# Optimization experiments

Hardware: AMD Instinct MI355X
Metric: run time of the kernel (lower is better)

## Reference

```python
import jax, jax.numpy as jnp
import numpy as np

B, N, D = 128, 64, 20
H, WM = 256, 4
CAUG = D + 1                      # time-augmented path channels
SIG = CAUG + CAUG * (CAUG - 1) // 2   # depth-2 log-signature channels = 231
C = SIG + 1                       # time-augmented control channels = 232
EPS = 1e-5


def _ln(x, g, b):
    m = jnp.mean(x, -1, keepdims=True)
    v = jnp.var(x, -1, keepdims=True)
    return (x - m) * jax.lax.rsqrt(v + EPS) * g + b


def setup_inputs():
    key = jax.random.key(0)
    ks = jax.random.split(key, 12)
    w = lambda k, s: (jax.random.normal(k, s) * 0.02).astype(jnp.float32)
    z = lambda s: jnp.zeros(s, jnp.float32)
    o = lambda s: jnp.ones(s, jnp.float32)
    return dict(
        x=jax.random.normal(ks[0], (B, N, D), jnp.float32),
        hW1=w(ks[1], (D, H)), hb1=z(H), hW2=w(ks[2], (H, H)), hb2=z(H),
        fW1=w(ks[3], (H, WM * H)), fb1=z(WM * H), g1=o(WM * H), be1=z(WM * H),
        fW2=w(ks[4], (WM * H, H)), fb2=z(H), g2=o(H), be2=z(H),
        fW3=w(ks[5], (H, H)), fb3=z(H),
        fW4=w(ks[6], (H, H * C)), fb4=z(H * C),
        yW1=w(ks[7], (H, H // 2)), yb1=z(H // 2), yW2=w(ks[8], (H // 2, 1)), yb2=z(1),
        zW1=w(ks[9], (H, H)), zb1=z(H), zW2=w(ks[10], (H, D)), zb2=z(D),
        sg=o(SIG), sb=z(SIG),
    )


def _forward(x, hW1, hb1, hW2, hb2, fW1, fb1, g1, be1, fW2, fb2, g2, be2,
             fW3, fb3, fW4, fb4, yW1, yb1, yW2, yb2, zW1, zb1, zW2, zb2, sg, sb):
    t = jnp.linspace(0.0, 1.0, N).astype(x.dtype)
    # --- depth-2 streamed log-signature of time-augmented path, basepoint 0 ---
    p = jnp.concatenate([jnp.broadcast_to(t[None, :, None], (B, N, 1)), x], -1)  # (B,N,CAUG)
    prev = jnp.concatenate([jnp.zeros((B, 1, CAUG), x.dtype), p[:, :-1]], 1)
    d = p - prev                                          # piecewise-linear segment increments
    term = prev[..., :, None] * d[..., None, :] - d[..., :, None] * prev[..., None, :]
    levy = 0.5 * jnp.cumsum(term, axis=1)                 # Levy areas, (B,N,CAUG,CAUG)
    iu, ju = np.triu_indices(CAUG, 1)
    logsig = jnp.concatenate([p, levy[:, :, iu, ju]], -1)  # level-1 + level-2 log-sig, (B,N,SIG)
    logsig = _ln(logsig, sg, sb)                          # sig_norm
    # --- natural cubic spline of time-augmented control ---
    y = jnp.concatenate([jnp.broadcast_to(t[None, :, None], (B, N, 1)), logsig], -1)  # (B,N,C)
    h = 1.0 / (N - 1)
    A = np.zeros((N, N), np.float32)
    A[0, 0] = A[-1, -1] = 1.0
    for i in range(1, N - 1):
        A[i, i - 1] = h / 6.0
        A[i, i] = 2.0 * h / 3.0
        A[i, i + 1] = h / 6.0
    rhs = jnp.concatenate([jnp.zeros((B, 1, C), y.dtype),
                           (y[:, 2:] - 2.0 * y[:, 1:-1] + y[:, :-2]) / h,
                           jnp.zeros((B, 1, C), y.dtype)], 1)
    M = jnp.linalg.solve(jnp.asarray(A), rhs.transpose(1, 0, 2).reshape(N, B * C))
    M = M.reshape(N, B, C).transpose(1, 0, 2)             # natural-spline second derivatives
    dy = (y[:, 1:] - y[:, :-1]) / h
    d_knot = dy - (h / 6.0) * (2.0 * M[:, :-1] + M[:, 1:])   # dX/dt at left knots, (B,N-1,C)
    d_mid = dy + (h / 24.0) * (M[:, :-1] - M[:, 1:])         # dX/dt at segment midpoints
    # --- initial hidden state ---
    h0 = jax.nn.relu(x[:, 0] @ hW1 + hb1) @ hW2 + hb2

    def vf(zz):  # RDEFunc MLP -> (B,H,C)
        a = jax.nn.relu(_ln(zz @ fW1 + fb1, g1, be1))
        a = jax.nn.relu(_ln(a @ fW2 + fb2, g2, be2))
        a = jax.nn.relu(a @ fW3 + fb3)
        return (a @ fW4 + fb4).reshape(B, H, C)

    def g(zz, dX):
        return jnp.einsum('bhc,bc->bh', vf(zz), dX)

    def step(zz, dd):  # explicit midpoint step of dz = F(z) dX/dt dt
        dk, dm = dd
        k1 = g(zz, dk)
        zn = zz + h * g(zz + 0.5 * h * k1, dm)
        return zn, zn

    _, hs = jax.lax.scan(step, h0, (d_knot.transpose(1, 0, 2), d_mid.transpose(1, 0, 2)))
    hT = hs[-1]                                            # terminal hidden (return_path=False)
    Y = jax.nn.relu(hT @ yW1 + yb1) @ yW2 + yb2
    Z = jax.nn.relu(hT @ zW1 + zb1) @ zW2 + zb2
    return Y, Z, hT


def reference(x, hW1, hb1, hW2, hb2, fW1, fb1, g1, be1, fW2, fb2, g2, be2,
              fW3, fb3, fW4, fb4, yW1, yb1, yW2, yb2, zW1, zb1, zW2, zb2, sg, sb):
    return _forward(x, hW1, hb1, hW2, hb2, fW1, fb1, g1, be1, fW2, fb2, g2, be2,
                    fW3, fb3, fW4, fb4, yW1, yb1, yW2, yb2, zW1, zb1, zW2, zb2, sg, sb)
```

## Files before the change

### kernel.cpp

```cpp
#include <hip/hip_runtime.h>

#define B 128
#define N 64
#define D 20
#define H 256
#define WMH 1024
#define CAUG 21
#define SIG 231
#define C 232
#define CP 240
#define KA 288
#define NSEG 63
#define NPH 126
#define HSTEP (1.0f/63.0f)
#define EPS 1e-5f

typedef __attribute__((ext_vector_type(8))) short short8;
typedef __attribute__((ext_vector_type(4))) float f32x4;
typedef __attribute__((ext_vector_type(4))) unsigned int uint4v;
typedef __attribute__((ext_vector_type(2))) int int2v;
typedef __attribute__((ext_vector_type(4))) int int4v;
typedef unsigned int uint;

__device__ inline short f2bf(float f) {
  uint u = __float_as_uint(f);
  uint r = (u + 0x7fffu + ((u >> 16) & 1u)) >> 16;
  return (short)r;
}
__device__ inline float bf2f(short h) {
  return __uint_as_float(((uint)(unsigned short)h) << 16);
}
#define MFMA16(a, b, c) __builtin_amdgcn_mfma_f32_16x16x32_bf16((a), (b), (c), 0, 0, 0)

__device__ inline void cstoreu(uint* p, uint v) {
  __hip_atomic_store(p, v, __ATOMIC_RELAXED, __HIP_MEMORY_SCOPE_AGENT);
}
__device__ inline void cstoref(float* p, float v) {
  __hip_atomic_store(p, v, __ATOMIC_RELAXED, __HIP_MEMORY_SCOPE_AGENT);
}
__device__ inline void cstorei(int* p, int v) {
  __hip_atomic_store(p, v, __ATOMIC_RELAXED, __HIP_MEMORY_SCOPE_AGENT);
}

#define CLOAD8(r0,r1,r2,r3,r4,r5,r6,r7,addr)                                   \
  asm volatile("global_load_dwordx4 %0, %8, off sc0 sc1\n\t"                   \
               "global_load_dwordx4 %1, %8, off offset:16 sc0 sc1\n\t"         \
               "global_load_dwordx4 %2, %8, off offset:128 sc0 sc1\n\t"        \
               "global_load_dwordx4 %3, %8, off offset:144 sc0 sc1\n\t"        \
               "global_load_dwordx4 %4, %8, off offset:256 sc0 sc1\n\t"        \
               "global_load_dwordx4 %5, %8, off offset:272 sc0 sc1\n\t"        \
               "global_load_dwordx4 %6, %8, off offset:384 sc0 sc1\n\t"        \
               "global_load_dwordx4 %7, %8, off offset:400 sc0 sc1\n\t"        \
               "s_waitcnt vmcnt(0)"                                            \
               : "=&v"(r0), "=&v"(r1), "=&v"(r2), "=&v"(r3),                   \
                 "=&v"(r4), "=&v"(r5), "=&v"(r6), "=&v"(r7)                    \
               : "v"(addr)                                                     \
               : "memory")

#define CLOAD2(r0,r1,addr)                                                     \
  asm volatile("global_load_dwordx4 %0, %2, off sc0 sc1\n\t"                   \
               "global_load_dwordx4 %1, %2, off offset:16 sc0 sc1\n\t"         \
               "s_waitcnt vmcnt(0)"                                            \
               : "=&v"(r0), "=&v"(r1) : "v"(addr) : "memory")

#define CLOADB2(r0,r1,a0,a1)                                                   \
  asm volatile("global_load_dwordx4 %0, %2, off sc0 sc1\n\t"                   \
               "global_load_dwordx4 %1, %3, off sc0 sc1\n\t"                   \
               "s_waitcnt vmcnt(0)"                                            \
               : "=&v"(r0), "=&v"(r1) : "v"(a0), "v"(a1) : "memory")

#define CLOAD9(r0,r1,r2,r3,r4,r5,r6,r7,r8,a0,a1,a2,a3,a4,a5,a6,a7,a8)          \
  asm volatile("global_load_dwordx4 %0, %9, off sc0 sc1\n\t"                   \
               "global_load_dwordx4 %1, %10, off sc0 sc1\n\t"                  \
               "global_load_dwordx4 %2, %11, off sc0 sc1\n\t"                  \
               "global_load_dwordx4 %3, %12, off sc0 sc1\n\t"                  \
               "global_load_dwordx4 %4, %13, off sc0 sc1\n\t"                  \
               "global_load_dwordx4 %5, %14, off sc0 sc1\n\t"                  \
               "global_load_dwordx4 %6, %15, off sc0 sc1\n\t"                  \
               "global_load_dwordx4 %7, %16, off sc0 sc1\n\t"                  \
               "global_load_dwordx4 %8, %17, off sc0 sc1\n\t"                  \
               "s_waitcnt vmcnt(0)"                                            \
               : "=&v"(r0), "=&v"(r1), "=&v"(r2), "=&v"(r3), "=&v"(r4),        \
                 "=&v"(r5), "=&v"(r6), "=&v"(r7), "=&v"(r8)                    \
               : "v"(a0), "v"(a1), "v"(a2), "v"(a3), "v"(a4), "v"(a5),         \
                 "v"(a6), "v"(a7), "v"(a8)                                     \
               : "memory")

__device__ inline void post(int* w, int v) {
  __builtin_amdgcn_fence(__ATOMIC_RELEASE, "workgroup");
  __syncthreads();
  if (threadIdx.x == 0) cstorei(w, v);
}
__device__ inline void poll16(const int* f, int tgt) {
  if (threadIdx.x < 64) {
    const int* p = f + (threadIdx.x & 15);
    for (;;) {
      int v;
      asm volatile("global_load_dword %0, %1, off sc0 sc1\n\ts_waitcnt vmcnt(0)"
                   : "=v"(v) : "v"(p) : "memory");
      if (__all(v >= tgt)) break;
      __builtin_amdgcn_s_sleep(1);
    }
  }
  __builtin_amdgcn_fence(__ATOMIC_ACQUIRE, "workgroup");
  __syncthreads();
}
__device__ inline void poll128(const int* f, int tgt) {
  if (threadIdx.x < 64) {
    const int* p = f + threadIdx.x * 2;
    for (;;) {
      int2v v;
      asm volatile("global_load_dwordx2 %0, %1, off sc0 sc1\n\ts_waitcnt vmcnt(0)"
                   : "=v"(v) : "v"(p) : "memory");
      if (__all(v[0] >= tgt && v[1] >= tgt)) break;
      __builtin_amdgcn_s_sleep(1);
    }
  }
  __builtin_amdgcn_fence(__ATOMIC_ACQUIRE, "workgroup");
  __syncthreads();
}
__device__ inline void poll256(const int* f, int tgt) {
  if (threadIdx.x < 64) {
    const int* p = f + threadIdx.x * 4;
    for (;;) {
      int4v v;
      asm volatile("global_load_dwordx4 %0, %1, off sc0 sc1\n\ts_waitcnt vmcnt(0)"
                   : "=v"(v) : "v"(p) : "memory");
      if (__all(v[0] >= tgt && v[1] >= tgt && v[2] >= tgt && v[3] >= tgt)) break;
      __builtin_amdgcn_s_sleep(1);
    }
  }
  __builtin_amdgcn_fence(__ATOMIC_ACQUIRE, "workgroup");
  __syncthreads();
}

__device__ inline void unpk(uint4v a, uint4v b, short8& ah, short8& al) {
#pragma unroll
  for (int e = 0; e < 4; e++) {
    ah[e]     = (short)(a[e] >> 16); al[e]     = (short)(a[e] & 0xffffu);
    ah[4 + e] = (short)(b[e] >> 16); al[4 + e] = (short)(b[e] & 0xffffu);
  }
}

__global__ __launch_bounds__(256) void k_logsig(const float* __restrict__ x,
                                                const float* __restrict__ sg,
                                                const float* __restrict__ sb,
                                                float* __restrict__ y) {
  __shared__ float yb[N][C];
  int b = blockIdx.x, tid = threadIdx.x;
  for (int ii = tid; ii < N * CAUG; ii += 256) {
    int n = ii / CAUG, j = ii % CAUG;
    float v = (j == 0) ? (n * (1.0f / 63.0f)) : x[(b * N + n) * D + (j - 1)];
    yb[n][1 + j] = v;
  }
  __syncthreads();
  if (tid < 210) {
    int i = 0, rem = tid;
    while (rem >= (CAUG - 1) - i) { rem -= (CAUG - 1) - i; i++; }
    int j = i + 1 + rem;
    float acc = 0.f, pi_prev = 0.f, pj_prev = 0.f;
    for (int n = 0; n < N; n++) {
      float pi = yb[n][1 + i], pj = yb[n][1 + j];
      float di = pi - pi_prev, dj = pj - pj_prev;
      acc += 0.5f * (pi_prev * dj - di * pj_prev);
      yb[n][1 + CAUG + tid] = acc;
      pi_prev = pi; pj_prev = pj;
    }
  }
  __syncthreads();
  int w = tid >> 6, l = tid & 63;
  for (int n = w; n < N; n += 4) {
    float s1 = 0.f, s2 = 0.f;
    for (int s = l; s < SIG; s += 64) { float v = yb[n][1 + s]; s1 += v; s2 += v * v; }
    for (int off = 32; off > 0; off >>= 1) { s1 += __shfl_down(s1, off); s2 += __shfl_down(s2, off); }
    s1 = __shfl(s1, 0); s2 = __shfl(s2, 0);
    float mean = s1 * (1.0f / SIG);
    float var  = s2 * (1.0f / SIG) - mean * mean;
    float rs = rsqrtf(var + EPS);
    float* yrow = y + ((size_t)b * N + n) * C;
    if (l == 0) yrow[0] = n * (1.0f / 63.0f);
    for (int s = l; s < SIG; s += 64)
      yrow[1 + s] = (yb[n][1 + s] - mean) * rs * sg[s] + sb[s];
  }
}

__global__ __launch_bounds__(256) void k_spline(const float* __restrict__ y,
                                                float* __restrict__ dknot,
                                                float* __restrict__ dmid) {
  __shared__ float yb[N * C];
  __shared__ float cp_s[62], id_s[62];
  int b = blockIdx.x, tid = threadIdx.x;
  for (int ii = tid; ii < N * C; ii += 256) yb[ii] = y[(size_t)b * N * C + ii];
  if (tid == 0) {
    const float a = HSTEP / 6.f, bb = 2.f * HSTEP / 3.f;
    float id0 = 1.f / bb; id_s[0] = id0; cp_s[0] = a * id0;
    for (int j = 1; j < 62; j++) {
      float den = bb - a * cp_s[j - 1];
      float idj = 1.f / den; id_s[j] = idj; cp_s[j] = a * idj;
    }
  }
  __syncthreads();
  int c = tid;
  if (c >= 232 && c < CP) {
    for (int n = 0; n < NSEG; n++) {
      dknot[((size_t)n * B + b) * CP + c] = 0.f;
      dmid [((size_t)n * B + b) * CP + c] = 0.f;
    }
  } else if (c < 232) {
    const float a = HSTEP / 6.f;
    float dp[62];
    dp[0] = (yb[2 * C + c] - 2.f * yb[1 * C + c] + yb[0 * C + c]) * 63.0f * id_s[0];
#pragma unroll
    for (int j = 1; j < 62; j++) {
      float rj = (yb[(j + 2) * C + c] - 2.f * yb[(j + 1) * C + c] + yb[j * C + c]) * 63.0f;
      dp[j] = (rj - a * dp[j - 1]) * id_s[j];
    }
#pragma unroll
    for (int j = 60; j >= 0; j--) dp[j] -= cp_s[j] * dp[j + 1];
#pragma unroll
    for (int n = 0; n < NSEG; n++) {
      float Mn  = (n == 0)  ? 0.f : dp[n - 1];
      float Mn1 = (n == 62) ? 0.f : dp[n];
      float dy = (yb[(n + 1) * C + c] - yb[n * C + c]) * 63.0f;
      dknot[((size_t)n * B + b) * CP + c] = dy - (HSTEP / 6.f)  * (2.f * Mn + Mn1);
      dmid [((size_t)n * B + b) * CP + c] = dy + (HSTEP / 24.f) * (Mn - Mn1);
    }
  }
}

__global__ __launch_bounds__(256) void k_h0(const float* __restrict__ x,
                                            const float* __restrict__ hW1,
                                            const float* __restrict__ hb1,
                                            const float* __restrict__ hW2,
                                            const float* __restrict__ hb2,
                                            float* __restrict__ z,
                                            uint* __restrict__ Xu) {
  __shared__ float r[H];
  int b = blockIdx.x, tid = threadIdx.x;
  float s = hb1[tid];
#pragma unroll
  for (int d = 0; d < D; d++) s += x[(size_t)(b * N) * D + d] * hW1[d * H + tid];
  r[tid] = fmaxf(s, 0.f);
  __syncthreads();
  float s2 = hb2[tid];
  for (int k = 0; k < H; k++) s2 += r[k] * hW2[k * H + tid];
  z[b * H + tid] = s2;
  short hi = f2bf(s2);
  short lo = f2bf(s2 - bf2f(hi));
  Xu[b * H + tid] = ((uint)(unsigned short)hi << 16) | (unsigned short)lo;
}

__global__ __launch_bounds__(256) void k_prep_t(const float* __restrict__ fW4,
                                                short* __restrict__ W4T) {
  __shared__ float tile[64][65];
  int m0 = blockIdx.x * 64, k0 = blockIdx.y * 64;
  int lane = threadIdx.x & 63, wr = threadIdx.x >> 6;
#pragma unroll
  for (int j = 0; j < 16; j++) {
    int kk = wr * 16 + j;
    tile[kk][lane] = fW4[(size_t)(k0 + kk) * 59392 + m0 + lane];
  }
  __syncthreads();
#pragma unroll
  for (int j = 0; j < 16; j++) {
    int mloc = wr * 16 + j;
    int m = m0 + mloc;
    int hh = m / 232, cc = m - hh * 232;
    W4T[((size_t)hh * CP + cc) * KA + k0 + lane] = f2bf(tile[lane][mloc]);
  }
}

__global__ __launch_bounds__(256) void k_prep_pad(const float* __restrict__ fb4,
                                                  short* __restrict__ W4T) {
  int idx = blockIdx.x * 256 + threadIdx.x;
  const int partA = 61440 * 32;
  if (idx < partA) {
    int row = idx >> 5, j = idx & 31;
    int hh = row / CP, cc = row - hh * CP;
    short v = 0;
    if (j == 0 && cc < 232) v = f2bf(fb4[hh * 232 + cc]);
    W4T[(size_t)row * KA + 256 + j] = v;
  } else {
    int t = idx - partA;
    int k = t & 255; t >>= 8;
    int cc = 232 + (t & 7); int hh = t >> 3;
    W4T[((size_t)hh * CP + cc) * KA + k] = 0;
  }
}

__global__ __launch_bounds__(256) void k_prep_wt(const float* __restrict__ in,
                                                 short* __restrict__ out,
                                                 int K, int Nn) {
  __shared__ float tile[64][65];
  int n0 = blockIdx.x * 64, k0 = blockIdx.y * 64;
  int lane = threadIdx.x & 63, wr = threadIdx.x >> 6;
#pragma unroll
  for (int j = 0; j < 16; j++) {
    int kk = wr * 16 + j;
    tile[kk][lane] = in[(size_t)(k0 + kk) * Nn + n0 + lane];
  }
  __syncthreads();
#pragma unroll
  for (int j = 0; j < 16; j++) {
    int nl = wr * 16 + j;
    out[(size_t)(n0 + nl) * K + k0 + lane] = f2bf(tile[lane][nl]);
  }
}

__global__ __launch_bounds__(128) void k_prep_t3pad(short* __restrict__ t3aug) {
  int r = threadIdx.x;
  if (r < 128) {
    int base = ((r >> 4) * 9 + 8) * 64 + (r & 15);
#pragma unroll
    for (int q = 0; q < 4; q++)
#pragma unroll
      for (int j = 0; j < 8; j++)
        t3aug[(size_t)(base + q * 16) * 8 + j] = (q == 0 && j == 0) ? (short)0x3F80 : (short)0;
  }
}

__global__ __launch_bounds__(256) void k_prep_zero(int* __restrict__ p, int n) {
  int i = blockIdx.x * 256 + threadIdx.x;
  if (i < n) p[i] = 0;
}

__global__ __launch_bounds__(512, 1) void k_scan(
    const short* __restrict__ W1T, const float* __restrict__ fb1,
    const float* __restrict__ g1,  const float* __restrict__ be1,
    const short* __restrict__ W2T, const float* __restrict__ fb2,
    const float* __restrict__ g2,  const float* __restrict__ be2,
    const short* __restrict__ W3T, const float* __restrict__ fb3,
    const short* __restrict__ W4T,
    const float* __restrict__ dknot, const float* __restrict__ dmid,
    float* __restrict__ z, uint* __restrict__ Xu, uint* __restrict__ t3u,
    float* __restrict__ T1, float* __restrict__ T2,
    int* __restrict__ flags) {
  const int blk = blockIdx.x;
  const int tid = threadIdx.x;
  const int wave = tid >> 6, lane = tid & 63;
  const int lm = lane & 15, q = lane >> 4;
  const int m = (blk & 127) >> 4;
  const int n = blk & 15;
  const int ks = wave >> 2, nwt = wave & 3;
  const int wv2 = (wave + n) & 7;
  const int wv3 = (wave + n) & 7;

  __shared__ short t3s[B * KA];
  __shared__ float red2[8][256];
  __shared__ float red4[8][128];
  __shared__ float zcol[128];
  __shared__ float g1s[WMH], be1s[WMH];
  __shared__ float g2s[H], be2s[H];
  __shared__ float fb1s[64];
  __shared__ float fb2s[16], fb3s[16];
  __shared__ uint xs[16 * 260];

  int* eS1 = flags;
  int* eS2 = flags + 128;
  int* eS3 = flags + 256;
  int* eS4 = flags + 384;

  const int nts = (wave < 7) ? 2 : 1;
  const int nt0 = wave * 2;
  short8 bfr[2][9];
  for (int t = 0; t < nts; t++) {
    const short* wp = W4T + ((size_t)blk * CP + (nt0 + t) * 16 + lm) * KA + q * 8;
#pragma unroll
    for (int kc = 0; kc < 9; kc++)
      bfr[t][kc] = *(const short8*)(wp + kc * 32);
  }
  short8 w1f[4], w2f[4], w3f;
  if (blk < 128) {
    const short* p1 = W1T + ((size_t)(n * 64 + nwt * 16 + lm)) * H + ks * 128 + q * 8;
#pragma unroll
    for (int kc = 0; kc < 4; kc++) w1f[kc] = *(const short8*)(p1 + kc * 32);
    const short* p2 = W2T + ((size_t)(n * 16 + lm)) * WMH + wv2 * 128 + q * 8;
#pragma unroll
    for (int kc = 0; kc < 4; kc++) w2f[kc] = *(const short8*)(p2 + kc * 32);
    w3f = *(const short8*)(W3T + ((size_t)(n * 16 + lm)) * H + wv3 * 32 + q * 8);
  }
  for (int i = tid; i < WMH; i += 512) { g1s[i] = g1[i]; be1s[i] = be1[i]; }
  for (int i = tid; i < H; i += 512)   { g2s[i] = g2[i]; be2s[i] = be2[i]; }
  if (tid < 64) fb1s[tid] = fb1[n * 64 + tid];
  if (tid < 16) { fb2s[tid] = fb2[n * 16 + tid]; fb3s[tid] = fb3[n * 16 + tid]; }
  if (tid < 128) zcol[tid] = z[(size_t)tid * H + blk];
  __syncthreads();

#pragma unroll 1
  for (int p = 0; p < NPH; p++) {
    const int seg = p >> 1, pm = p & 1;
    const float* dX = (pm ? dmid : dknot) + (size_t)seg * B * CP;
    const float scale = pm ? HSTEP : 0.5f * HSTEP;

    if (blk < 128) {
      if (p) poll256(eS4, p);
      {
        const uint* xsrc = Xu + (size_t)(m * 16) * H;
        int j0 = tid * 4, j1 = (tid + 512) * 4;
        uint4v v0, v1;
        CLOADB2(v0, v1, xsrc + j0, xsrc + j1);
        *(uint4v*)&xs[(j0 >> 8) * 260 + (j0 & 255)] = v0;
        *(uint4v*)&xs[(j1 >> 8) * 260 + (j1 & 255)] = v1;
      }
      __syncthreads();
      {
        f32x4 acc = {0.f, 0.f, 0.f, 0.f};
        const int xb = lm * 260 + ks * 128 + q * 8;
#pragma unroll
        for (int kc = 0; kc < 4; kc++) {
          uint4v a = *(const uint4v*)&xs[xb + kc * 32];
          uint4v b = *(const uint4v*)&xs[xb + kc * 32 + 4];
          short8 ah, al;
          unpk(a, b, ah, al);
          acc = MFMA16(ah, w1f[kc], acc);
          acc = MFMA16(al, w1f[kc], acc);
        }
#pragma unroll
        for (int r = 0; r < 4; r++) red2[wave][(q * 4 + r) * 16 + lm] = acc[r];
      }
      __syncthreads();
      if (wave < 4) {
        int col = n * 64 + wave * 16 + lm;
        float fb = fb1s[wave * 16 + lm];
#pragma unroll
        for (int r = 0; r < 4; r++) {
          int idx = (q * 4 + r) * 16 + lm;
          float v = red2[wave][idx] + red2[wave + 4][idx] + fb;
          cstoref(T1 + (size_t)(m * 16 + q * 4 + r) * WMH + col, v);
        }
      }
      post(eS1 + m * 16 + n, p + 1);

      poll16(eS1 + m * 16, p + 1);
      const float* tp = T1 + (size_t)(m * 16 + lm) * WMH + wv2 * 128 + q * 8;
      uint4v yv[8];
      CLOAD8(yv[0], yv[1], yv[2], yv[3], yv[4], yv[5], yv[6], yv[7], tp);
      {
        float s = 0.f, ss = 0.f;
#pragma unroll
        for (int i = 0; i < 8; i++)
#pragma unroll
          for (int e = 0; e < 4; e++) {
            float v = __uint_as_float(yv[i][e]);
            s += v; ss += v * v;
          }
        s += __shfl_xor(s, 16); ss += __shfl_xor(ss, 16);
        s += __shfl_xor(s, 32); ss += __shfl_xor(ss, 32);
        if (q == 0) { red2[wave][lm] = s; red2[wave][16 + lm] = ss; }
        __syncthreads();
        float S = 0.f, SS = 0.f;
#pragma unroll
        for (int w = 0; w < 8; w++) { S += red2[w][lm]; SS += red2[w][16 + lm]; }
        float mean = S * (1.f / WMH);
        float var  = SS * (1.f / WMH) - mean * mean;
        float rsv  = rsqrtf(var + EPS);
        __syncthreads();
        f32x4 acc = {0.f, 0.f, 0.f, 0.f};
#pragma unroll
        for (int kc = 0; kc < 4; kc++) {
          int kg = wv2 * 128 + kc * 32 + q * 8;
          short8 ah, al;
#pragma unroll
          for (int jj = 0; jj < 8; jj++) {
            float v = __uint_as_float(yv[kc * 2 + (jj >> 2)][jj & 3]);
            float a = fmaxf((v - mean) * rsv * g1s[kg + jj] + be1s[kg + jj], 0.f);
            short hi = f2bf(a);
            ah[jj] = hi;
            al[jj] = f2bf(a - bf2f(hi));
          }
          acc = MFMA16(ah, w2f[kc], acc);
          acc = MFMA16(al, w2f[kc], acc);
        }
#pragma unroll
        for (int r = 0; r < 4; r++) red2[wave][(q * 4 + r) * 16 + lm] = acc[r];
      }
      __syncthreads();
      if (tid < 256) {
        int ri = tid >> 4, ci = tid & 15;
        float v = fb2s[ci];
#pragma unroll
        for (int w = 0; w < 8; w++) v += red2[w][tid];
        cstoref(T2 + (size_t)(m * 16 + ri) * H + n * 16 + ci, v);
      }
      post(eS2 + m * 16 + n, p + 1);

      poll16(eS2 + m * 16, p + 1);
      const float* t2p = T2 + (size_t)(m * 16 + lm) * H + wv3 * 32 + q * 8;
      uint4v u0, u1;
      CLOAD2(u0, u1, t2p);
      {
        float s = 0.f, ss = 0.f;
#pragma unroll
        for (int e = 0; e < 4; e++) {
          float v0 = __uint_as_float(u0[e]), v1 = __uint_as_float(u1[e]);
          s += v0 + v1; ss += v0 * v0 + v1 * v1;
        }
        s += __shfl_xor(s, 16); ss += __shfl_xor(ss, 16);
        s += __shfl_xor(s, 32); ss += __shfl_xor(ss, 32);
        if (q == 0) { red2[wave][lm] = s; red2[wave][16 + lm] = ss; }
        __syncthreads();
        float S = 0.f, SS = 0.f;
#pragma unroll
        for (int w = 0; w < 8; w++) { S += red2[w][lm]; SS += red2[w][16 + lm]; }
        float mean = S * (1.f / H);
        float var  = SS * (1.f / H) - mean * mean;
        float rsv  = rsqrtf(var + EPS);
        __syncthreads();
        int kg = wv3 * 32 + q * 8;
        short8 ah, al;
#pragma unroll
        for (int jj = 0; jj < 8; jj++) {
          float v = __uint_as_float((jj < 4 ? u0[jj & 3] : u1[jj & 3]));
          float a = fmaxf((v - mean) * rsv * g2s[kg + jj] + be2s[kg + jj], 0.f);
          short hi = f2bf(a);
          ah[jj] = hi;
          al[jj] = f2bf(a - bf2f(hi));
        }
        f32x4 acc = {0.f, 0.f, 0.f, 0.f};
        acc = MFMA16(ah, w3f, acc);
        acc = MFMA16(al, w3f, acc);
#pragma unroll
        for (int r = 0; r < 4; r++) red2[wave][(q * 4 + r) * 16 + lm] = acc[r];
      }
      __syncthreads();
      if (tid < 256) {
        int ri = tid >> 4, ci = tid & 15;
        float v = fb3s[ci];
#pragma unroll
        for (int w = 0; w < 8; w++) v += red2[w][tid];
        v = fmaxf(v, 0.f);
        float vo = __shfl_xor(v, 1);
        if ((ci & 1) == 0) {
          int kglob = n * 16 + ci;
          int d = (m * 9 + (kglob >> 5)) * 64 + ((kglob >> 3) & 3) * 16 + ri;
          uint u = ((uint)(unsigned short)f2bf(vo) << 16)
                 | (unsigned short)f2bf(v);
          cstoreu(t3u + d * 4 + ((kglob & 7) >> 1), u);
        }
      }
      post(eS3 + m * 16 + n, p + 1);
    } else {
      if (p + 1 < NPH) {
        const int seg2 = (p + 1) >> 1, pm2 = (p + 1) & 1;
        const float* dX2 = (pm2 ? dmid : dknot) + (size_t)seg2 * B * CP;
        int i0 = tid * 64;
        if (i0 > B * CP - 64) i0 = B * CP - 64;
        int i1 = i0 + 32;
        float t0, t1;
        asm volatile("global_load_dword %0, %2, off\n\t"
                     "global_load_dword %1, %3, off\n\t"
                     "s_waitcnt vmcnt(0)"
                     : "=&v"(t0), "=&v"(t1)
                     : "v"(dX2 + i0), "v"(dX2 + i1) : "memory");
        asm volatile("" :: "v"(t0), "v"(t1));
      }
    }

    {
      poll128(eS3, p + 1);
      {
        int s0 = blk % 9;
        int s1 = s0 + 1 >= 9 ? s0 + 1 - 9 : s0 + 1;
        int s2 = s1 + 1 >= 9 ? s1 + 1 - 9 : s1 + 1;
        int s3 = s2 + 1 >= 9 ? s2 + 1 - 9 : s2 + 1;
        int s4 = s3 + 1 >= 9 ? s3 + 1 - 9 : s3 + 1;
        int s5 = s4 + 1 >= 9 ? s4 + 1 - 9 : s4 + 1;
        int s6 = s5 + 1 >= 9 ? s5 + 1 - 9 : s5 + 1;
        int s7 = s6 + 1 >= 9 ? s6 + 1 - 9 : s6 + 1;
        int s8 = s7 + 1 >= 9 ? s7 + 1 - 9 : s7 + 1;
        const uint* tb = t3u + tid * 4;
        uint4v r0, r1, r2, r3, r4, r5, r6, r7, r8;
        CLOAD9(r0, r1, r2, r3, r4, r5, r6, r7, r8,
               tb + s0 * 2048, tb + s1 * 2048, tb + s2 * 2048,
               tb + s3 * 2048, tb + s4 * 2048, tb + s5 * 2048,
               tb + s6 * 2048, tb + s7 * 2048, tb + s8 * 2048);
        *(uint4v*)(t3s + (size_t)s0 * 4096 + tid * 8) = r0;
        *(uint4v*)(t3s + (size_t)s1 * 4096 + tid * 8) = r1;
        *(uint4v*)(t3s + (size_t)s2 * 4096 + tid * 8) = r2;
        *(uint4v*)(t3s + (size_t)s3 * 4096 + tid * 8) = r3;
        *(uint4v*)(t3s + (size_t)s4 * 4096 + tid * 8) = r4;
        *(uint4v*)(t3s + (size_t)s5 * 4096 + tid * 8) = r5;
        *(uint4v*)(t3s + (size_t)s6 * 4096 + tid * 8) = r6;
        *(uint4v*)(t3s + (size_t)s7 * 4096 + tid * 8) = r7;
        *(uint4v*)(t3s + (size_t)s8 * 4096 + tid * 8) = r8;
      }
      __syncthreads();
      for (int mm = 0; mm < 8; mm++) {
        short8 afr[9];
#pragma unroll
        for (int kc = 0; kc < 9; kc++)
          afr[kc] = *(const short8*)(t3s + (size_t)((mm * 9 + kc) * 64 + lane) * 8);
        f32x4 acc0 = {0.f, 0.f, 0.f, 0.f}, acc1 = {0.f, 0.f, 0.f, 0.f};
#pragma unroll
        for (int kc = 0; kc < 9; kc++) {
          acc0 = MFMA16(afr[kc], bfr[0][kc], acc0);
          if (nts > 1) acc1 = MFMA16(afr[kc], bfr[1][kc], acc1);
        }
        float part[4];
#pragma unroll
        for (int r = 0; r < 4; r++) {
          int row = mm * 16 + q * 4 + r;
          float pv = acc0[r] * dX[(size_t)row * CP + nt0 * 16 + lm];
          if (nts > 1) pv += acc1[r] * dX[(size_t)row * CP + (nt0 + 1) * 16 + lm];
          part[r] = pv;
        }
#pragma unroll
        for (int r = 0; r < 4; r++) {
          part[r] += __shfl_xor(part[r], 1);
          part[r] += __shfl_xor(part[r], 2);
          part[r] += __shfl_xor(part[r], 4);
          part[r] += __shfl_xor(part[r], 8);
        }
        if (lm == 0) {
#pragma unroll
          for (int r = 0; r < 4; r++) red4[wave][mm * 16 + q * 4 + r] = part[r];
        }
      }
      __syncthreads();
      if (tid < 128) {
        int row = tid;
        float s = 0.f;
#pragma unroll
        for (int w = 0; w < 8; w++) s += red4[w][row];
        float zo = zcol[row] + scale * s;
        if (pm) zcol[row] = zo;
        if (p == NPH - 1) z[(size_t)row * H + blk] = zo;
        short hi = f2bf(zo);
        short lo = f2bf(zo - bf2f(hi));
        cstoreu(Xu + (size_t)row * H + blk,
                ((uint)(unsigned short)hi << 16) | (unsigned short)lo);
      }
      post(eS4 + blk, p + 1);
    }
  }
}

__global__ __launch_bounds__(256) void k_final(const float* __restrict__ z,
    const float* __restrict__ yW1, const float* __restrict__ yb1,
    const float* __restrict__ yW2, const float* __restrict__ yb2,
    const float* __restrict__ zW1, const float* __restrict__ zb1,
    const float* __restrict__ zW2, const float* __restrict__ zb2,
    float* __restrict__ out) {
  __shared__ float ht[H];
  __shared__ float ry[128];
  __shared__ float rz[H];
  int b = blockIdx.x, tid = threadIdx.x;
  ht[tid] = z[(size_t)b * H + tid];
  __syncthreads();
  if (tid < 128) {
    float s = yb1[tid];
    for (int k = 0; k < H; k++) s += ht[k] * yW1[k * 128 + tid];
    ry[tid] = fmaxf(s, 0.f);
  }
  {
    float s = zb1[tid];
    for (int k = 0; k < H; k++) s += ht[k] * zW1[k * H + tid];
    rz[tid] = fmaxf(s, 0.f);
  }
  __syncthreads();
  if (tid < 64) {
    float sv = ry[tid] * yW2[tid] + ry[tid + 64] * yW2[tid + 64];
    for (int off = 32; off > 0; off >>= 1) sv += __shfl_down(sv, off);
    if (tid == 0) out[b] = sv + yb2[0];
  }
  if (tid < D) {
    float s = zb2[tid];
    for (int k = 0; k < H; k++) s += rz[k] * zW2[k * D + tid];
    out[B + b * D + tid] = s;
  }
  out[B + B * D + (size_t)b * H + tid] = ht[tid];
}

extern "C" void kernel_launch(void* const* d_in, const int* in_sizes, int n_in,
                              void* d_out, int out_size, void* d_ws, size_t ws_size,
                              hipStream_t stream) {
  const float* x   = (const float*)d_in[0];
  const float* hW1 = (const float*)d_in[1];
  const float* hb1 = (const float*)d_in[2];
  const float* hW2 = (const float*)d_in[3];
  const float* hb2 = (const float*)d_in[4];
  const float* fW1 = (const float*)d_in[5];
  const float* fb1 = (const float*)d_in[6];
  const float* g1  = (const float*)d_in[7];
  const float* be1 = (const float*)d_in[8];
  const float* fW2 = (const float*)d_in[9];
  const float* fb2 = (const float*)d_in[10];
  const float* g2  = (const float*)d_in[11];
  const float* be2 = (const float*)d_in[12];
  const float* fW3 = (const float*)d_in[13];
  const float* fb3 = (const float*)d_in[14];
  const float* fW4 = (const float*)d_in[15];
  const float* fb4 = (const float*)d_in[16];
  const float* yW1 = (const float*)d_in[17];
  const float* yb1 = (const float*)d_in[18];
  const float* yW2 = (const float*)d_in[19];
  const float* yb2 = (const float*)d_in[20];
  const float* zW1 = (const float*)d_in[21];
  const float* zb1 = (const float*)d_in[22];
  const float* zW2 = (const float*)d_in[23];
  const float* zb2 = (const float*)d_in[24];
  const float* sg  = (const float*)d_in[25];
  const float* sb  = (const float*)d_in[26];

  float* ws     = (float*)d_ws;
  float* dknot  = ws;
  float* dmid   = dknot + (size_t)NSEG * B * CP;
  float* z      = dmid + (size_t)NSEG * B * CP;
  float* T1     = z + B * H;
  float* T2     = T1 + B * WMH;
  uint* Xu      = (uint*)(T2 + B * H);
  uint* t3u     = Xu + B * H;
  int* flags    = (int*)(t3u + B * KA / 2);
  short* w1T    = (short*)(flags + 1024);
  short* w2T    = w1T + H * WMH;
  short* w3T    = w2T + H * WMH;
  short* W4T    = w3T + H * H;
  float* y      = (float*)W4T;

  hipLaunchKernelGGL(k_logsig, dim3(B), dim3(256), 0, stream, x, sg, sb, y);
  hipLaunchKernelGGL(k_spline, dim3(B), dim3(256), 0, stream, y, dknot, dmid);
  hipLaunchKernelGGL(k_h0,     dim3(B), dim3(256), 0, stream, x, hW1, hb1, hW2, hb2, z, Xu);
  hipLaunchKernelGGL(k_prep_t,   dim3(928, 4), dim3(256), 0, stream, fW4, W4T);
  hipLaunchKernelGGL(k_prep_pad, dim3(9728),   dim3(256), 0, stream, fb4, W4T);
  hipLaunchKernelGGL(k_prep_wt,  dim3(16, 4),  dim3(256), 0, stream, fW1, w1T, H, WMH);
  hipLaunchKernelGGL(k_prep_wt,  dim3(4, 16),  dim3(256), 0, stream, fW2, w2T, WMH, H);
  hipLaunchKernelGGL(k_prep_wt,  dim3(4, 4),   dim3(256), 0, stream, fW3, w3T, H, H);
  hipLaunchKernelGGL(k_prep_t3pad, dim3(1), dim3(128), 0, stream, (short*)t3u);
  hipLaunchKernelGGL(k_prep_zero, dim3(4), dim3(256), 0, stream, flags, 1024);

  void* args[] = {
    (void*)&w1T, (void*)&fb1, (void*)&g1, (void*)&be1,
    (void*)&w2T, (void*)&fb2, (void*)&g2, (void*)&be2,
    (void*)&w3T, (void*)&fb3, (void*)&W4T,
    (void*)&dknot, (void*)&dmid,
    (void*)&z, (void*)&Xu, (void*)&t3u,
    (void*)&T1, (void*)&T2, (void*)&flags
  };
  hipLaunchCooperativeKernel((const void*)k_scan, dim3(256), dim3(512), args, 0, stream);

  hipLaunchKernelGGL(k_final, dim3(B), dim3(256), 0, stream, z,
                     yW1, yb1, yW2, yb2, zW1, zb1, zW2, zb2, (float*)d_out);
}
```

Measured before the change: 3.787 ms.

## Keep FC1 tile in LDS, exchange LayerNorm stats and split-K FC2 via atomics

Each block now keeps its 16x64 slice of the first MLP layer in shared memory instead of writing the full T1 activation to global memory. Blocks publish only per-row partial sums and sums of squares for the LayerNorm, and compute the second layer as a split-K over their own 64 columns, accumulating into a double-buffered global T2 with relaxed atomic adds. The aim is to remove the global T1 round trip and the redundant 1024-wide reads per block in the serial scan. In exchange it adds float atomics, whose accumulation order is nondeterministic, plus a zeroing pass for the T2 buffer that relies on the double buffering and flag ordering being correct.

```diff
diff --git a/kernel.cpp b/kernel.cpp
--- a/kernel.cpp
+++ b/kernel.cpp
@@ -41,21 +41,15 @@
 __device__ inline void cstorei(int* p, int v) {
   __hip_atomic_store(p, v, __ATOMIC_RELAXED, __HIP_MEMORY_SCOPE_AGENT);
 }
-
-#define CLOAD8(r0,r1,r2,r3,r4,r5,r6,r7,addr)                                   \
-  asm volatile("global_load_dwordx4 %0, %8, off sc0 sc1\n\t"                   \
-               "global_load_dwordx4 %1, %8, off offset:16 sc0 sc1\n\t"         \
-               "global_load_dwordx4 %2, %8, off offset:128 sc0 sc1\n\t"        \
-               "global_load_dwordx4 %3, %8, off offset:144 sc0 sc1\n\t"        \
-               "global_load_dwordx4 %4, %8, off offset:256 sc0 sc1\n\t"        \
-               "global_load_dwordx4 %5, %8, off offset:272 sc0 sc1\n\t"        \
-               "global_load_dwordx4 %6, %8, off offset:384 sc0 sc1\n\t"        \
-               "global_load_dwordx4 %7, %8, off offset:400 sc0 sc1\n\t"        \
-               "s_waitcnt vmcnt(0)"                                            \
-               : "=&v"(r0), "=&v"(r1), "=&v"(r2), "=&v"(r3),                   \
-                 "=&v"(r4), "=&v"(r5), "=&v"(r6), "=&v"(r7)                    \
-               : "v"(addr)                                                     \
-               : "memory")
+__device__ inline void catomadd(float* p, float v) {
+  (void)__hip_atomic_fetch_add(p, v, __ATOMIC_RELAXED, __HIP_MEMORY_SCOPE_AGENT);
+}
+__device__ inline float cloadf(const float* p) {
+  float v;
+  asm volatile("global_load_dword %0, %1, off sc0 sc1\n\ts_waitcnt vmcnt(0)"
+               : "=v"(v) : "v"(p) : "memory");
+  return v;
+}
 
 #define CLOAD2(r0,r1,addr)                                                     \
   asm volatile("global_load_dwordx4 %0, %2, off sc0 sc1\n\t"                   \
@@ -333,7 +327,7 @@
     const short* __restrict__ W4T,
     const float* __restrict__ dknot, const float* __restrict__ dmid,
     float* __restrict__ z, uint* __restrict__ Xu, uint* __restrict__ t3u,
-    float* __restrict__ T1, float* __restrict__ T2,
+    float* __restrict__ T2d, float* __restrict__ statsG,
     int* __restrict__ flags) {
   const int blk = blockIdx.x;
   const int tid = threadIdx.x;
@@ -342,7 +336,6 @@
   const int m = (blk & 127) >> 4;
   const int n = blk & 15;
   const int ks = wave >> 2, nwt = wave & 3;
-  const int wv2 = (wave + n) & 7;
   const int wv3 = (wave + n) & 7;
 
   __shared__ short t3s[B * KA];
@@ -352,8 +345,11 @@
   __shared__ float g1s[WMH], be1s[WMH];
   __shared__ float g2s[H], be2s[H];
   __shared__ float fb1s[64];
-  __shared__ float fb2s[16], fb3s[16];
+  __shared__ float fb2F[H];
+  __shared__ float fb3s[16];
   __shared__ uint xs[16 * 260];
+  __shared__ float t1s[16][68];
+  __shared__ float fstat[32];
 
   int* eS1 = flags;
   int* eS2 = flags + 128;
@@ -369,20 +365,24 @@
     for (int kc = 0; kc < 9; kc++)
       bfr[t][kc] = *(const short8*)(wp + kc * 32);
   }
-  short8 w1f[4], w2f[4], w3f;
+  short8 w1f[4], w2n[2][2], w3f;
   if (blk < 128) {
     const short* p1 = W1T + ((size_t)(n * 64 + nwt * 16 + lm)) * H + ks * 128 + q * 8;
 #pragma unroll
     for (int kc = 0; kc < 4; kc++) w1f[kc] = *(const short8*)(p1 + kc * 32);
-    const short* p2 = W2T + ((size_t)(n * 16 + lm)) * WMH + wv2 * 128 + q * 8;
-#pragma unroll
-    for (int kc = 0; kc < 4; kc++) w2f[kc] = *(const short8*)(p2 + kc * 32);
+#pragma unroll
+    for (int t = 0; t < 2; t++)
+#pragma unroll
+      for (int kc2 = 0; kc2 < 2; kc2++)
+        w2n[t][kc2] = *(const short8*)(W2T +
+            ((size_t)(wave * 32 + t * 16 + lm)) * WMH + n * 64 + kc2 * 32 + q * 8);
     w3f = *(const short8*)(W3T + ((size_t)(n * 16 + lm)) * H + wv3 * 32 + q * 8);
   }
   for (int i = tid; i < WMH; i += 512) { g1s[i] = g1[i]; be1s[i] = be1[i]; }
   for (int i = tid; i < H; i += 512)   { g2s[i] = g2[i]; be2s[i] = be2[i]; }
   if (tid < 64) fb1s[tid] = fb1[n * 64 + tid];
-  if (tid < 16) { fb2s[tid] = fb2[n * 16 + tid]; fb3s[tid] = fb3[n * 16 + tid]; }
+  if (tid < H) fb2F[tid] = fb2[tid];
+  if (tid < 16) fb3s[tid] = fb3[n * 16 + tid];
   if (tid < 128) zcol[tid] = z[(size_t)tid * H + blk];
   __syncthreads();
 
@@ -391,6 +391,7 @@
     const int seg = p >> 1, pm = p & 1;
     const float* dX = (pm ? dmid : dknot) + (size_t)seg * B * CP;
     const float scale = pm ? HSTEP : 0.5f * HSTEP;
+    float* T2cur = T2d + (size_t)(p & 1) * (B * H);
 
     if (blk < 128) {
       if (p) poll256(eS4, p);
@@ -420,72 +421,79 @@
       }
       __syncthreads();
       if (wave < 4) {
-        int col = n * 64 + wave * 16 + lm;
-        float fb = fb1s[wave * 16 + lm];
 #pragma unroll
         for (int r = 0; r < 4; r++) {
           int idx = (q * 4 + r) * 16 + lm;
-          float v = red2[wave][idx] + red2[wave + 4][idx] + fb;
-          cstoref(T1 + (size_t)(m * 16 + q * 4 + r) * WMH + col, v);
+          t1s[q * 4 + r][wave * 16 + lm] =
+              red2[wave][idx] + red2[wave + 4][idx] + fb1s[wave * 16 + lm];
+        }
+      }
+      __syncthreads();
+      if (tid < 256) {
+        int row = tid >> 4, cg = tid & 15;
+        float s = 0.f, ss = 0.f;
+#pragma unroll
+        for (int j = 0; j < 4; j++) {
+          float v = t1s[row][cg * 4 + j];
+          s += v; ss += v * v;
+        }
+        s += __shfl_xor(s, 1); ss += __shfl_xor(ss, 1);
+        s += __shfl_xor(s, 2); ss += __shfl_xor(ss, 2);
+        s += __shfl_xor(s, 4); ss += __shfl_xor(ss, 4);
+        s += __shfl_xor(s, 8); ss += __shfl_xor(ss, 8);
+        if (cg == 0) {
+          cstoref(statsG + (size_t)(m * 16 + n) * 32 + row * 2, s);
+          cstoref(statsG + (size_t)(m * 16 + n) * 32 + row * 2 + 1, ss);
         }
       }
       post(eS1 + m * 16 + n, p + 1);
 
       poll16(eS1 + m * 16, p + 1);
-      const float* tp = T1 + (size_t)(m * 16 + lm) * WMH + wv2 * 128 + q * 8;
-      uint4v yv[8];
-      CLOAD8(yv[0], yv[1], yv[2], yv[3], yv[4], yv[5], yv[6], yv[7], tp);
+      ((float*)red2)[tid] = cloadf(statsG + (size_t)m * 512 + tid);
+      __syncthreads();
+      if (tid < 32) {
+        float s = 0.f;
+#pragma unroll
+        for (int nn = 0; nn < 16; nn++) s += ((float*)red2)[nn * 32 + tid];
+        fstat[tid] = s;
+      }
+      __syncthreads();
       {
-        float s = 0.f, ss = 0.f;
-#pragma unroll
-        for (int i = 0; i < 8; i++)
-#pragma unroll
-          for (int e = 0; e < 4; e++) {
-            float v = __uint_as_float(yv[i][e]);
-            s += v; ss += v * v;
-          }
-        s += __shfl_xor(s, 16); ss += __shfl_xor(ss, 16);
-        s += __shfl_xor(s, 32); ss += __shfl_xor(ss, 32);
-        if (q == 0) { red2[wave][lm] = s; red2[wave][16 + lm] = ss; }
-        __syncthreads();
-        float S = 0.f, SS = 0.f;
-#pragma unroll
-        for (int w = 0; w < 8; w++) { S += red2[w][lm]; SS += red2[w][16 + lm]; }
-        float mean = S * (1.f / WMH);
-        float var  = SS * (1.f / WMH) - mean * mean;
+        float mean = fstat[lm * 2] * (1.f / WMH);
+        float var  = fstat[lm * 2 + 1] * (1.f / WMH) - mean * mean;
         float rsv  = rsqrtf(var + EPS);
-        __syncthreads();
-        f32x4 acc = {0.f, 0.f, 0.f, 0.f};
-#pragma unroll
-        for (int kc = 0; kc < 4; kc++) {
-          int kg = wv2 * 128 + kc * 32 + q * 8;
+        f32x4 acc0 = {0.f, 0.f, 0.f, 0.f}, acc1 = {0.f, 0.f, 0.f, 0.f};
+#pragma unroll
+        for (int kc2 = 0; kc2 < 2; kc2++) {
+          const float* tp = &t1s[lm][kc2 * 32 + q * 8];
           short8 ah, al;
 #pragma unroll
           for (int jj = 0; jj < 8; jj++) {
-            float v = __uint_as_float(yv[kc * 2 + (jj >> 2)][jj & 3]);
-            float a = fmaxf((v - mean) * rsv * g1s[kg + jj] + be1s[kg + jj], 0.f);
+            int gcol = n * 64 + kc2 * 32 + q * 8 + jj;
+            float a = fmaxf((tp[jj] - mean) * rsv * g1s[gcol] + be1s[gcol], 0.f);
             short hi = f2bf(a);
             ah[jj] = hi;
             al[jj] = f2bf(a - bf2f(hi));
           }
-          acc = MFMA16(ah, w2f[kc], acc);
-          acc = MFMA16(al, w2f[kc], acc);
-        }
-#pragma unroll
-        for (int r = 0; r < 4; r++) red2[wave][(q * 4 + r) * 16 + lm] = acc[r];
-      }
-      __syncthreads();
-      if (tid < 256) {
-        int ri = tid >> 4, ci = tid & 15;
-        float v = fb2s[ci];
-#pragma unroll
-        for (int w = 0; w < 8; w++) v += red2[w][tid];
-        cstoref(T2 + (size_t)(m * 16 + ri) * H + n * 16 + ci, v);
+          acc0 = MFMA16(ah, w2n[0][kc2], acc0);
+          acc0 = MFMA16(al, w2n[0][kc2], acc0);
+          acc1 = MFMA16(ah, w2n[1][kc2], acc1);
+          acc1 = MFMA16(al, w2n[1][kc2], acc1);
+        }
+#pragma unroll
+        for (int r = 0; r < 4; r++) {
+          int row = m * 16 + q * 4 + r;
+          int c0 = wave * 32 + lm;
+          float v0 = acc0[r], v1 = acc1[r];
+          if (n == 0) { v0 += fb2F[c0]; v1 += fb2F[c0 + 16]; }
+          catomadd(T2cur + (size_t)row * H + c0, v0);
+          catomadd(T2cur + (size_t)row * H + c0 + 16, v1);
+        }
       }
       post(eS2 + m * 16 + n, p + 1);
 
       poll16(eS2 + m * 16, p + 1);
-      const float* t2p = T2 + (size_t)(m * 16 + lm) * H + wv3 * 32 + q * 8;
+      const float* t2p = T2cur + (size_t)(m * 16 + lm) * H + wv3 * 32 + q * 8;
       uint4v u0, u1;
       CLOAD2(u0, u1, t2p);
       {
@@ -558,6 +566,10 @@
 
     {
       poll128(eS3, p + 1);
+      if (blk < 128 && tid < 256) {
+        int ri = tid >> 4, ci = tid & 15;
+        cstoref(T2cur + (size_t)(m * 16 + ri) * H + n * 16 + ci, 0.f);
+      }
       {
         int s0 = blk % 9;
         int s1 = s0 + 1 >= 9 ? s0 + 1 - 9 : s0 + 1;
@@ -706,9 +718,9 @@
   float* dknot  = ws;
   float* dmid   = dknot + (size_t)NSEG * B * CP;
   float* z      = dmid + (size_t)NSEG * B * CP;
-  float* T1     = z + B * H;
-  float* T2     = T1 + B * WMH;
-  uint* Xu      = (uint*)(T2 + B * H);
+  float* T2d    = z + B * H;
+  float* statsG = T2d + (size_t)2 * B * H;
+  uint* Xu      = (uint*)(statsG + 4096);
   uint* t3u     = Xu + B * H;
   int* flags    = (int*)(t3u + B * KA / 2);
   short* w1T    = (short*)(flags + 1024);
@@ -727,6 +739,7 @@
   hipLaunchKernelGGL(k_prep_wt,  dim3(4, 4),   dim3(256), 0, stream, fW3, w3T, H, H);
   hipLaunchKernelGGL(k_prep_t3pad, dim3(1), dim3(128), 0, stream, (short*)t3u);
   hipLaunchKernelGGL(k_prep_zero, dim3(4), dim3(256), 0, stream, flags, 1024);
+  hipLaunchKernelGGL(k_prep_zero, dim3(256), dim3(256), 0, stream, (int*)T2d, 2 * B * H);
 
   void* args[] = {
     (void*)&w1T, (void*)&fb1, (void*)&g1, (void*)&be1,
@@ -734,7 +747,7 @@
     (void*)&w3T, (void*)&fb3, (void*)&W4T,
     (void*)&dknot, (void*)&dmid,
     (void*)&z, (void*)&Xu, (void*)&t3u,
-    (void*)&T1, (void*)&T2, (void*)&flags
+    (void*)&T2d, (void*)&statsG, (void*)&flags
   };
   hipLaunchCooperativeKernel((const void*)k_scan, dim3(256), dim3(512), args, 0, stream);
 
```

Result: faster. 3.697 ms (-2.4%).
